# Kernel tuning notes

Hardware: AMD Instinct MI355X
Metric: run time of the kernel (lower is better)

The kernel has to match this reference:

```python
import jax, jax.numpy as jnp
import numpy as np

B, T, K, V, D, H = 16, 512, 32, 512, 64, 128


def setup_inputs() -> dict:
    key = jax.random.key(0)
    ks = jax.random.split(key, 10)
    s = lambda k, shape: jax.random.normal(k, shape, jnp.float32) * 0.05
    sequences = jax.random.randint(ks[0], (B, T), 0, V)
    lengths = jax.random.randint(ks[1], (B,), 1, T + 1)
    return dict(
        sequences=sequences,
        lengths=lengths,
        emb=s(ks[2], (V, D)),
        W1=s(ks[3], (D, H)), b1=jnp.zeros((H,), jnp.float32),
        W2=s(ks[4], (H, K * K)), b2=jnp.zeros((K * K,), jnp.float32),
        E1=s(ks[5], (D, H)), e1=jnp.zeros((H,), jnp.float32),
        E2=s(ks[6], (H, K * V)), e2=jnp.zeros((K * V,), jnp.float32),
        init_logits=s(ks[7], (K,)),
    )


def reference(sequences, lengths, emb, W1, b1, W2, b2, E1, e1, E2, e2, init_logits):
    Bc, Tc = sequences.shape
    # shift inputs: start token 0 followed by sequences[:, :-1]
    inputs = jnp.concatenate(
        [jnp.zeros((Bc, 1), sequences.dtype), sequences[:, :-1]], axis=1)
    x = emb[inputs]                                  # (B,T,D)
    # transition net -> (B,T,K,K) row-normalized in log space
    h1 = jax.nn.relu(x @ W1 + b1)
    log_trans = jax.nn.log_softmax((h1 @ W2 + b2).reshape(Bc, Tc, K, K), axis=-1)
    # emission net -> (B,T,K,V), gather observed-token scores
    h2 = jax.nn.relu(x @ E1 + e1)
    log_emit = jax.nn.log_softmax((h2 @ E2 + e2).reshape(Bc, Tc, K, V), axis=-1)
    tgt = jnp.broadcast_to(sequences[:, :, None, None], (Bc, Tc, K, 1))
    emit_scores = jnp.take_along_axis(log_emit, tgt, axis=3)[..., 0]  # (B,T,K)
    init_lp = jax.nn.log_softmax(init_logits)
    alpha0 = init_lp[None, :] + emit_scores[:, 0]    # (B,K)

    def step(alpha, xs):
        lt, es, t = xs                               # (B,K,K),(B,K),()
        new = jax.nn.logsumexp(alpha[:, :, None] + lt, axis=1) + es
        alpha = jnp.where((t < lengths)[:, None], new, alpha)
        return alpha, None

    xs = (jnp.swapaxes(log_trans, 0, 1)[1:],
          jnp.swapaxes(emit_scores, 0, 1)[1:],
          jnp.arange(1, Tc))
    alpha, _ = jax.lax.scan(step, alpha0, xs)
    return -jax.nn.logsumexp(alpha, axis=1)         # (B,) negative log-likelihood
```

## Files before the change

kernel.cpp:

```cpp
#include <hip/hip_runtime.h>
#include <hip/hip_bf16.h>

#define BB 16
#define TT 512
#define KK 32
#define VV 512
#define DD 64
#define HH 128
#define KV (KK*VV)
#define KKK (KK*KK)

#define INV_LN2 1.4426950408889634f
#define LN2 0.6931471805599453f

typedef unsigned short u16;
typedef __attribute__((ext_vector_type(8))) short short8;
typedef __attribute__((ext_vector_type(8))) unsigned short ushort8;
typedef __attribute__((ext_vector_type(16))) float f32x16;
typedef __attribute__((ext_vector_type(4))) unsigned int uint4v;

__device__ __forceinline__ float fexp2(float x) { return __builtin_amdgcn_exp2f(x); }
__device__ __forceinline__ float flog2(float x) { return __builtin_amdgcn_logf(x); }

__device__ __forceinline__ u16 f2bf(float f) {
  unsigned u = __builtin_bit_cast(unsigned, f);
  u += 0x7FFFu + ((u >> 16) & 1u);
  return (u16)(u >> 16);
}
__device__ __forceinline__ float bf2f(u16 v) {
  return __builtin_bit_cast(float, ((unsigned)v) << 16);
}

__device__ __forceinline__ float es_dot(const u16* __restrict__ erow,
                                        const u16* __restrict__ hrow) {
  float dot = 0.f;
#pragma unroll
  for (int r = 0; r < 8; ++r) {
    short8 ev = ((const short8*)erow)[r];
    short8 hv = ((const short8*)hrow)[r];
#pragma unroll
    for (int e = 0; e < 8; ++e)
      dot += bf2f((u16)ev[e]) * bf2f((u16)hv[e]);
  }
  return dot;
}

__device__ __forceinline__ void mul_step(short8 fr0, short8 fr1, int h,
                                         float* D) {
  float e0[8], e1[8];
#pragma unroll
  for (int i2 = 0; i2 < 4; ++i2) {
    float x0 = __shfl_xor(D[i2], 32);
    float y0 = __shfl_xor(D[4 + i2], 32);
    e0[i2] = (h == 0) ? D[i2] : y0;
    e0[4 + i2] = (h == 0) ? x0 : D[4 + i2];
    float x1 = __shfl_xor(D[8 + i2], 32);
    float y1 = __shfl_xor(D[12 + i2], 32);
    e1[i2] = (h == 0) ? D[8 + i2] : y1;
    e1[4 + i2] = (h == 0) ? x1 : D[12 + i2];
  }
  short8 B0, B1;
#pragma unroll
  for (int e = 0; e < 8; ++e) {
    B0[e] = (short)f2bf(e0[e]);
    B1[e] = (short)f2bf(e1[e]);
  }
  f32x16 dn = {};
  dn = __builtin_amdgcn_mfma_f32_32x32x16_bf16(fr0, B0, dn, 0, 0, 0);
  dn = __builtin_amdgcn_mfma_f32_32x32x16_bf16(fr1, B1, dn, 0, 0, 0);
#pragma unroll
  for (int r = 0; r < 16; ++r) D[r] = dn[r];
}

__device__ __forceinline__ void ident_D(int j, int h, float* D) {
#pragma unroll
  for (int r = 0; r < 16; ++r) D[r] = 0.f;
  if (((j >> 2) & 1) == h) D[(j & 3) | ((j >> 3) << 2)] = 1.0f;
}

__global__ __launch_bounds__(256) void k_prep(
    const float* __restrict__ E2, u16* __restrict__ E2bT,
    const float* __restrict__ emb, const float* __restrict__ W1,
    const float* __restrict__ b1, const float* __restrict__ E1,
    const float* __restrict__ e1, const float* __restrict__ W2,
    const float* __restrict__ b2, float* __restrict__ ltrans,
    u16* __restrict__ h2b) {
  __shared__ float tl[32][65];
  __shared__ float embs[4][64];
  __shared__ float h1s[4][128];
  __shared__ float lg[4][32 * 33];
  __shared__ float lsev[4][32];
  int tid = threadIdx.x;

  if (blockIdx.x < 1024) {
    int c0 = (blockIdx.x & 255) * 64, h0 = (blockIdx.x >> 8) * 32;
    int r = tid >> 6, c = tid & 63;
#pragma unroll
    for (int rr = 0; rr < 8; ++rr)
      tl[r * 8 + rr][c] = E2[(size_t)(h0 + r * 8 + rr) * KV + c0 + c];
    __syncthreads();
    int cw = tid >> 3, hb = tid & 7;
#pragma unroll
    for (int pass = 0; pass < 2; ++pass) {
      int cc = pass * 32 + cw;
      unsigned lo = (unsigned)f2bf(tl[hb * 4 + 0][cc]) |
                    ((unsigned)f2bf(tl[hb * 4 + 1][cc]) << 16);
      unsigned hi = (unsigned)f2bf(tl[hb * 4 + 2][cc]) |
                    ((unsigned)f2bf(tl[hb * 4 + 3][cc]) << 16);
      uint2 v;
      v.x = lo;
      v.y = hi;
      *(uint2*)(E2bT + (size_t)(c0 + cc) * HH + h0 + hb * 4) = v;
    }
    return;
  }

  int u0 = (blockIdx.x - 1024) * 4;
  {
    int tok = tid >> 6, d = tid & 63;
    embs[tok][d] = emb[(u0 + tok) * DD + d];
  }
  __syncthreads();
#pragma unroll
  for (int p = 0; p < 2; ++p) {
    int tok = p * 2 + (tid >> 7), hh = tid & 127;
    float a1 = b1[hh], a2 = e1[hh];
#pragma unroll 8
    for (int d = 0; d < DD; ++d) {
      float xv = embs[tok][d];
      a1 += xv * W1[d * HH + hh];
      a2 += xv * E1[d * HH + hh];
    }
    h1s[tok][hh] = fmaxf(a1, 0.f);
    h2b[(u0 + tok) * HH + hh] = f2bf(fmaxf(a2, 0.f));
  }
  __syncthreads();
  float acc[4][4];
#pragma unroll
  for (int r = 0; r < 4; ++r) {
    float bb = b2[tid + r * 256];
#pragma unroll
    for (int tok = 0; tok < 4; ++tok) acc[tok][r] = bb;
  }
#pragma unroll 2
  for (int hh = 0; hh < HH; ++hh) {
    float w0 = W2[hh * KKK + tid];
    float w1 = W2[hh * KKK + tid + 256];
    float w2v = W2[hh * KKK + tid + 512];
    float w3 = W2[hh * KKK + tid + 768];
#pragma unroll
    for (int tok = 0; tok < 4; ++tok) {
      float hv = h1s[tok][hh];
      acc[tok][0] += hv * w0;
      acc[tok][1] += hv * w1;
      acc[tok][2] += hv * w2v;
      acc[tok][3] += hv * w3;
    }
  }
#pragma unroll
  for (int tok = 0; tok < 4; ++tok)
#pragma unroll
    for (int r = 0; r < 4; ++r) {
      int cc = tid + r * 256;
      lg[tok][(cc >> 5) * 33 + (cc & 31)] = acc[tok][r] * INV_LN2;
    }
  __syncthreads();
  if (tid < 128) {
    int tok = tid >> 5, i = tid & 31;
    float m = -1e30f;
    for (int jj = 0; jj < KK; ++jj) m = fmaxf(m, lg[tok][i * 33 + jj]);
    float s = 0.f;
    for (int jj = 0; jj < KK; ++jj) s += fexp2(lg[tok][i * 33 + jj] - m);
    lsev[tok][i] = m + flog2(s);
  }
  __syncthreads();
#pragma unroll
  for (int tok = 0; tok < 4; ++tok)
#pragma unroll
    for (int r = 0; r < 4; ++r) {
      int cc = tid + r * 256;
      int jj = cc >> 5, ii = cc & 31;
      ltrans[(u0 + tok) * KKK + jj * KK + ii] =
          lg[tok][ii * 33 + jj] - lsev[tok][ii];
    }
}

__global__ __launch_bounds__(256) void k_emit_lse(
    const u16* __restrict__ h2b, const u16* __restrict__ E2bT,
    const float* __restrict__ e2, float* __restrict__ lse2_tab) {
  int k = blockIdx.x;
  int u0 = blockIdx.y * 32;
  int tid = threadIdx.x;
  int w = tid >> 6, l = tid & 63;
  int h = l >> 5, j = l & 31;
  __shared__ float ls[4 * 32];

  short8 A[8];
#pragma unroll
  for (int kh = 0; kh < 8; ++kh)
    A[kh] = *(const short8*)(h2b + (u0 + j) * HH + kh * 16 + h * 8);

  float s[16];
#pragma unroll
  for (int r = 0; r < 16; ++r) s[r] = 0.f;

#pragma unroll
  for (int c = 0; c < 4; ++c) {
    int ct = w * 4 + c;
    int col = k * 512 + ct * 32 + j;
    const u16* bp = E2bT + (size_t)col * HH + h * 8;
    f32x16 acc = {};
#pragma unroll
    for (int kh = 0; kh < 8; ++kh) {
      short8 Bf = *(const short8*)(bp + kh * 16);
      acc = __builtin_amdgcn_mfma_f32_32x32x16_bf16(A[kh], Bf, acc, 0, 0, 0);
    }
    float e2v = e2[col] * INV_LN2;
#pragma unroll
    for (int r = 0; r < 16; ++r) s[r] += fexp2(acc[r] * INV_LN2 + e2v);
  }
#pragma unroll
  for (int r = 0; r < 16; ++r) {
#pragma unroll
    for (int d = 1; d < 32; d <<= 1) s[r] += __shfl_xor(s[r], d);
  }
  if (j == 0) {
#pragma unroll
    for (int r = 0; r < 16; ++r) {
      int row = (r & 3) + 8 * (r >> 2) + 4 * h;
      ls[w * 32 + row] = s[r];
    }
  }
  __syncthreads();
  if (tid < 32) {
    float total = ls[tid] + ls[32 + tid] + ls[64 + tid] + ls[96 + tid];
    lse2_tab[(u0 + tid) * KK + k] = flog2(total);
  }
}

__global__ __launch_bounds__(256) void k_matprod(
    const int* __restrict__ seq, const int* __restrict__ lengths,
    const float* __restrict__ ltrans, const u16* __restrict__ h2b,
    const u16* __restrict__ E2bT, const float* __restrict__ e2,
    const float* __restrict__ lse2, u16* __restrict__ C1,
    float* __restrict__ s1) {
  __shared__ float tmp[4][32 * 33];
  int w = threadIdx.x >> 6, l = threadIdx.x & 63;
  int c = blockIdx.x * 4 + w;
  int b = c >> 6, t0 = (c & 63) * 8;
  int j = l & 31, h = l >> 5;
  int len = lengths[b];
  len = (len < 1) ? 1 : ((len > TT) ? TT : len);
  const int* sb = seq + b * TT;
  int tlo = (t0 < 1) ? 1 : t0;
  int thi = (t0 + 8 < len) ? (t0 + 8) : len;

  u16* op = C1 + (size_t)c * 1024 + j * 32 + h * 16;
  if (tlo >= thi) {
    ushort8 w0v, w1v;
#pragma unroll
    for (int e = 0; e < 8; ++e) {
      w0v[e] = ((h * 16 + e) == j) ? (u16)0x3F80 : (u16)0;
      w1v[e] = ((h * 16 + 8 + e) == j) ? (u16)0x3F80 : (u16)0;
    }
    *(ushort8*)op = w0v;
    *(ushort8*)(op + 8) = w1v;
    if (l == 0) s1[c] = 0.f;
    return;
  }

  short8 fr0s[8], fr1s[8];
  float sacc = 0.f;
#pragma unroll
  for (int s = 0; s < 8; ++s) {
    int t = t0 + s;
    if (t >= 1 && t < len) {
      int u = sb[t - 1], y = sb[t];
      float dot = es_dot(E2bT + (size_t)(j * VV + y) * HH + h * 64,
                         h2b + u * HH + h * 64);
      dot += __shfl_xor(dot, 32);
      float esj = (dot + e2[j * VV + y]) * INV_LN2 - lse2[u * KK + j];
      float m = esj;
#pragma unroll
      for (int d = 1; d < 32; d <<= 1) m = fmaxf(m, __shfl_xor(m, d));
      sacc += m;
      const float4* p4 = (const float4*)(ltrans + u * KKK + j * KK + h * 16);
      float4 q0 = p4[0], q1 = p4[1], q2 = p4[2], q3 = p4[3];
      float lgv[16] = {q0.x, q0.y, q0.z, q0.w, q1.x, q1.y, q1.z, q1.w,
                       q2.x, q2.y, q2.z, q2.w, q3.x, q3.y, q3.z, q3.w};
      float off = esj - m;
#pragma unroll
      for (int e = 0; e < 16; ++e) lgv[e] += off;
      unsigned pk[8];
#pragma unroll
      for (int p = 0; p < 8; ++p)
        pk[p] = (unsigned)f2bf(fexp2(lgv[2 * p])) |
                ((unsigned)f2bf(fexp2(lgv[2 * p + 1])) << 16);
      unsigned rcv[4];
#pragma unroll
      for (int p = 0; p < 4; ++p)
        rcv[p] = (unsigned)__shfl_xor((int)(h == 0 ? pk[4 + p] : pk[p]), 32);
      unsigned f0[4], f1[4];
#pragma unroll
      for (int p = 0; p < 4; ++p) {
        f0[p] = h == 0 ? pk[p] : rcv[p];
        f1[p] = h == 0 ? rcv[p] : pk[4 + p];
      }
      fr0s[s] = __builtin_bit_cast(short8, (uint4v){f0[0], f0[1], f0[2], f0[3]});
      fr1s[s] = __builtin_bit_cast(short8, (uint4v){f1[0], f1[1], f1[2], f1[3]});
    } else {
      ushort8 i0, i1;
#pragma unroll
      for (int e = 0; e < 8; ++e) {
        i0[e] = ((h * 8 + e) == j) ? (u16)0x3F80 : (u16)0;
        i1[e] = ((16 + h * 8 + e) == j) ? (u16)0x3F80 : (u16)0;
      }
      fr0s[s] = __builtin_bit_cast(short8, i0);
      fr1s[s] = __builtin_bit_cast(short8, i1);
    }
  }

  float D[16];
  ident_D(j, h, D);
#pragma unroll
  for (int s = 0; s < 8; ++s) mul_step(fr0s[s], fr1s[s], h, D);

  float mx = D[0];
#pragma unroll
  for (int r = 1; r < 16; ++r) mx = fmaxf(mx, D[r]);
#pragma unroll
  for (int d = 1; d < 64; d <<= 1) mx = fmaxf(mx, __shfl_xor(mx, d));
  float inv = 1.0f / mx;
#pragma unroll
  for (int r = 0; r < 16; ++r) {
    int row = (r & 3) + 8 * (r >> 2) + 4 * h;
    tmp[w][row * 33 + j] = D[r] * inv;
  }
  ushort8 w0v, w1v;
#pragma unroll
  for (int e = 0; e < 8; ++e) {
    w0v[e] = f2bf(tmp[w][j * 33 + h * 16 + e]);
    w1v[e] = f2bf(tmp[w][j * 33 + h * 16 + 8 + e]);
  }
  *(ushort8*)op = w0v;
  *(ushort8*)(op + 8) = w1v;
  if (l == 0) s1[c] = flog2(mx) + sacc;
}

__global__ __launch_bounds__(512) void k_final2(
    const u16* __restrict__ C1, const float* __restrict__ s1,
    const int* __restrict__ seq, const u16* __restrict__ h2b,
    const u16* __restrict__ E2bT, const float* __restrict__ e2,
    const float* __restrict__ lse2, const float* __restrict__ init_logits,
    float* __restrict__ out) {
  __shared__ u16 mats[8][1024];
  __shared__ float scs[8];
  int b = blockIdx.x;
  int w = threadIdx.x >> 6, l = threadIdx.x & 63;
  int j = l & 31, h = l >> 5;

  float D[16];
  ident_D(j, h, D);
  const u16* base = C1 + ((size_t)b * 64 + w * 8) * 1024;
#pragma unroll
  for (int s = 0; s < 8; ++s) {
    short8 fr0 = *(const short8*)(base + s * 1024 + j * 32 + h * 8);
    short8 fr1 = *(const short8*)(base + s * 1024 + j * 32 + h * 8 + 16);
    mul_step(fr0, fr1, h, D);
  }
  float mx = D[0];
#pragma unroll
  for (int r = 1; r < 16; ++r) mx = fmaxf(mx, D[r]);
#pragma unroll
  for (int d = 1; d < 64; d <<= 1) mx = fmaxf(mx, __shfl_xor(mx, d));
  float inv = 1.0f / mx;
#pragma unroll
  for (int r = 0; r < 16; ++r) {
    int row = (r & 3) + 8 * (r >> 2) + 4 * h;
    mats[w][row * 32 + j] = f2bf(D[r] * inv);
  }
  float si = (l < 8) ? s1[b * 64 + w * 8 + l] : 0.f;
#pragma unroll
  for (int d = 1; d < 64; d <<= 1) si += __shfl_xor(si, d);
  if (l == 0) scs[w] = flog2(mx) + si;
  __syncthreads();

  if (w == 0) {
    float D2[16];
    ident_D(j, h, D2);
#pragma unroll
    for (int s = 0; s < 8; ++s) {
      short8 fr0 = *(const short8*)(&mats[s][j * 32 + h * 8]);
      short8 fr1 = *(const short8*)(&mats[s][j * 32 + h * 8 + 16]);
      mul_step(fr0, fr1, h, D2);
    }
    int y0 = seq[b * TT];
    float dot = es_dot(E2bT + (size_t)(j * VV + y0) * HH + h * 64,
                       h2b + h * 64);
    dot += __shfl_xor(dot, 32);
    float esj = (dot + e2[j * VV + y0]) * INV_LN2 - lse2[j];
    float il = init_logits[j] * INV_LN2;
    float m0 = il;
#pragma unroll
    for (int d = 1; d < 32; d <<= 1) m0 = fmaxf(m0, __shfl_xor(m0, d));
    float s0 = fexp2(il - m0);
#pragma unroll
    for (int d = 1; d < 32; d <<= 1) s0 += __shfl_xor(s0, d);
    float lse0 = m0 + flog2(s0);
    float z = il - lse0 + esj;
    float am = z;
#pragma unroll
    for (int d = 1; d < 32; d <<= 1) am = fmaxf(am, __shfl_xor(am, d));
    float a0 = fexp2(z - am);
    float colsum = 0.f;
#pragma unroll
    for (int r = 0; r < 16; ++r) colsum += D2[r];
    float p = a0 * colsum;
#pragma unroll
    for (int d = 1; d < 64; d <<= 1) p += __shfl_xor(p, d);
    float sct = (l < 8) ? scs[l] : 0.f;
#pragma unroll
    for (int d = 1; d < 64; d <<= 1) sct += __shfl_xor(sct, d);
    if (l == 0) out[b] = -LN2 * (flog2(p) + am + sct);
  }
}

extern "C" void kernel_launch(void* const* d_in, const int* in_sizes, int n_in,
                              void* d_out, int out_size, void* d_ws,
                              size_t ws_size, hipStream_t stream) {
  const int* seq = (const int*)d_in[0];
  const int* lengths = (const int*)d_in[1];
  const float* emb = (const float*)d_in[2];
  const float* W1 = (const float*)d_in[3];
  const float* b1 = (const float*)d_in[4];
  const float* W2 = (const float*)d_in[5];
  const float* b2 = (const float*)d_in[6];
  const float* E1 = (const float*)d_in[7];
  const float* e1 = (const float*)d_in[8];
  const float* E2 = (const float*)d_in[9];
  const float* e2 = (const float*)d_in[10];
  const float* init_logits = (const float*)d_in[11];
  float* out = (float*)d_out;

  char* wsb = (char*)d_ws;
  float* ltrans = (float*)(wsb + 0);
  u16* h2b = (u16*)(wsb + 2097152);
  u16* E2bT = (u16*)(wsb + 2228224);
  float* lse2 = (float*)(wsb + 6422528);
  u16* C1 = (u16*)(wsb + 6488064);
  float* s1 = (float*)(wsb + 8585216);

  k_prep<<<1152, 256, 0, stream>>>(E2, E2bT, emb, W1, b1, E1, e1, W2, b2,
                                   ltrans, h2b);
  k_emit_lse<<<dim3(32, 16), 256, 0, stream>>>(h2b, E2bT, e2, lse2);
  k_matprod<<<256, 256, 0, stream>>>(seq, lengths, ltrans, h2b, E2bT, e2,
                                     lse2, C1, s1);
  k_final2<<<16, 512, 0, stream>>>(C1, s1, seq, h2b, E2bT, e2, lse2,
                                   init_logits, out);
}
```

Measured before the change: 88.56 us.

## Compute transition logits with MFMA and rebalance matprod chunk length

The fp32 scalar W2 projection and log-softmax in the prep kernel are replaced by a new MFMA kernel working on bf16 h1 and a transposed bf16 W2, with the row log-sum-exp done through wave shuffles. The prep kernel now also transposes W2 and processes 16 tokens per block for the first-layer MLPs. The matprod chunk shrinks from 8 to 4 steps, doubling its blocks, while the final kernel multiplies 16 chunk matrices per wave instead of 8. The es_dot reduction gains four independent accumulators. In exchange this adds a kernel launch, lowers transition precision to bf16 inputs, and lengthens the serial chain in the final kernel.

```diff
diff --git a/kernel.cpp b/kernel.cpp
--- a/kernel.cpp
+++ b/kernel.cpp
@@ -33,16 +33,21 @@
 
 __device__ __forceinline__ float es_dot(const u16* __restrict__ erow,
                                         const u16* __restrict__ hrow) {
-  float dot = 0.f;
+  float a0 = 0.f, a1 = 0.f, a2 = 0.f, a3 = 0.f;
 #pragma unroll
   for (int r = 0; r < 8; ++r) {
     short8 ev = ((const short8*)erow)[r];
     short8 hv = ((const short8*)hrow)[r];
-#pragma unroll
-    for (int e = 0; e < 8; ++e)
-      dot += bf2f((u16)ev[e]) * bf2f((u16)hv[e]);
-  }
-  return dot;
+    a0 += bf2f((u16)ev[0]) * bf2f((u16)hv[0]);
+    a1 += bf2f((u16)ev[1]) * bf2f((u16)hv[1]);
+    a2 += bf2f((u16)ev[2]) * bf2f((u16)hv[2]);
+    a3 += bf2f((u16)ev[3]) * bf2f((u16)hv[3]);
+    a0 += bf2f((u16)ev[4]) * bf2f((u16)hv[4]);
+    a1 += bf2f((u16)ev[5]) * bf2f((u16)hv[5]);
+    a2 += bf2f((u16)ev[6]) * bf2f((u16)hv[6]);
+    a3 += bf2f((u16)ev[7]) * bf2f((u16)hv[7]);
+  }
+  return (a0 + a1) + (a2 + a3);
 }
 
 __device__ __forceinline__ void mul_step(short8 fr0, short8 fr1, int h,
@@ -78,26 +83,41 @@
   if (((j >> 2) & 1) == h) D[(j & 3) | ((j >> 3) << 2)] = 1.0f;
 }
 
-__global__ __launch_bounds__(256) void k_prep(
+__global__ __launch_bounds__(256) void k_prep1(
     const float* __restrict__ E2, u16* __restrict__ E2bT,
+    const float* __restrict__ W2, u16* __restrict__ W2T,
     const float* __restrict__ emb, const float* __restrict__ W1,
     const float* __restrict__ b1, const float* __restrict__ E1,
-    const float* __restrict__ e1, const float* __restrict__ W2,
-    const float* __restrict__ b2, float* __restrict__ ltrans,
+    const float* __restrict__ e1, u16* __restrict__ h1b,
     u16* __restrict__ h2b) {
   __shared__ float tl[32][65];
-  __shared__ float embs[4][64];
-  __shared__ float h1s[4][128];
-  __shared__ float lg[4][32 * 33];
-  __shared__ float lsev[4][32];
+  __shared__ float embs[16][64];
   int tid = threadIdx.x;
-
-  if (blockIdx.x < 1024) {
-    int c0 = (blockIdx.x & 255) * 64, h0 = (blockIdx.x >> 8) * 32;
+  int bid = blockIdx.x;
+
+  if (bid < 1088) {
+    const float* src;
+    u16* dst;
+    size_t srcld;
+    int c0, h0;
+    if (bid < 1024) {
+      c0 = (bid & 255) * 64;
+      h0 = (bid >> 8) * 32;
+      src = E2;
+      dst = E2bT;
+      srcld = KV;
+    } else {
+      int b2i = bid - 1024;
+      c0 = (b2i & 15) * 64;
+      h0 = (b2i >> 4) * 32;
+      src = W2;
+      dst = W2T;
+      srcld = KKK;
+    }
     int r = tid >> 6, c = tid & 63;
 #pragma unroll
     for (int rr = 0; rr < 8; ++rr)
-      tl[r * 8 + rr][c] = E2[(size_t)(h0 + r * 8 + rr) * KV + c0 + c];
+      tl[r * 8 + rr][c] = src[(size_t)(h0 + r * 8 + rr) * srcld + c0 + c];
     __syncthreads();
     int cw = tid >> 3, hb = tid & 7;
 #pragma unroll
@@ -110,79 +130,68 @@
       uint2 v;
       v.x = lo;
       v.y = hi;
-      *(uint2*)(E2bT + (size_t)(c0 + cc) * HH + h0 + hb * 4) = v;
+      *(uint2*)(dst + (size_t)(c0 + cc) * HH + h0 + hb * 4) = v;
     }
     return;
   }
 
-  int u0 = (blockIdx.x - 1024) * 4;
-  {
-    int tok = tid >> 6, d = tid & 63;
-    embs[tok][d] = emb[(u0 + tok) * DD + d];
+  int u0 = (bid - 1088) * 16;
+#pragma unroll
+  for (int it = 0; it < 4; ++it) {
+    int idx = it * 256 + tid;
+    embs[idx >> 6][idx & 63] = emb[u0 * DD + idx];
   }
   __syncthreads();
-#pragma unroll
-  for (int p = 0; p < 2; ++p) {
-    int tok = p * 2 + (tid >> 7), hh = tid & 127;
-    float a1 = b1[hh], a2 = e1[hh];
+  int h = tid & 127, tl2 = tid >> 7;
+  float b1v = b1[h], e1v = e1[h];
+#pragma unroll
+  for (int it = 0; it < 8; ++it) {
+    int tok = it * 2 + tl2;
+    float a1 = b1v, a2 = e1v;
 #pragma unroll 8
     for (int d = 0; d < DD; ++d) {
       float xv = embs[tok][d];
-      a1 += xv * W1[d * HH + hh];
-      a2 += xv * E1[d * HH + hh];
-    }
-    h1s[tok][hh] = fmaxf(a1, 0.f);
-    h2b[(u0 + tok) * HH + hh] = f2bf(fmaxf(a2, 0.f));
-  }
-  __syncthreads();
-  float acc[4][4];
-#pragma unroll
-  for (int r = 0; r < 4; ++r) {
-    float bb = b2[tid + r * 256];
-#pragma unroll
-    for (int tok = 0; tok < 4; ++tok) acc[tok][r] = bb;
-  }
-#pragma unroll 2
-  for (int hh = 0; hh < HH; ++hh) {
-    float w0 = W2[hh * KKK + tid];
-    float w1 = W2[hh * KKK + tid + 256];
-    float w2v = W2[hh * KKK + tid + 512];
-    float w3 = W2[hh * KKK + tid + 768];
-#pragma unroll
-    for (int tok = 0; tok < 4; ++tok) {
-      float hv = h1s[tok][hh];
-      acc[tok][0] += hv * w0;
-      acc[tok][1] += hv * w1;
-      acc[tok][2] += hv * w2v;
-      acc[tok][3] += hv * w3;
-    }
-  }
-#pragma unroll
-  for (int tok = 0; tok < 4; ++tok)
-#pragma unroll
-    for (int r = 0; r < 4; ++r) {
-      int cc = tid + r * 256;
-      lg[tok][(cc >> 5) * 33 + (cc & 31)] = acc[tok][r] * INV_LN2;
-    }
-  __syncthreads();
-  if (tid < 128) {
-    int tok = tid >> 5, i = tid & 31;
-    float m = -1e30f;
-    for (int jj = 0; jj < KK; ++jj) m = fmaxf(m, lg[tok][i * 33 + jj]);
-    float s = 0.f;
-    for (int jj = 0; jj < KK; ++jj) s += fexp2(lg[tok][i * 33 + jj] - m);
-    lsev[tok][i] = m + flog2(s);
-  }
-  __syncthreads();
-#pragma unroll
-  for (int tok = 0; tok < 4; ++tok)
-#pragma unroll
-    for (int r = 0; r < 4; ++r) {
-      int cc = tid + r * 256;
-      int jj = cc >> 5, ii = cc & 31;
-      ltrans[(u0 + tok) * KKK + jj * KK + ii] =
-          lg[tok][ii * 33 + jj] - lsev[tok][ii];
-    }
+      a1 += xv * W1[d * HH + h];
+      a2 += xv * E1[d * HH + h];
+    }
+    h1b[(u0 + tok) * HH + h] = f2bf(fmaxf(a1, 0.f));
+    h2b[(u0 + tok) * HH + h] = f2bf(fmaxf(a2, 0.f));
+  }
+}
+
+__global__ __launch_bounds__(256) void k_transmfma(
+    const u16* __restrict__ h1b, const u16* __restrict__ W2T,
+    const float* __restrict__ b2, float* __restrict__ ltrans) {
+  int i = blockIdx.x;
+  int w = threadIdx.x >> 6, l = threadIdx.x & 63;
+  int tt = blockIdx.y * 4 + w;
+  int u0 = tt * 32;
+  int h = l >> 5, j = l & 31;
+
+  f32x16 acc = {};
+#pragma unroll
+  for (int kh = 0; kh < 8; ++kh) {
+    short8 A = *(const short8*)(h1b + (u0 + j) * HH + kh * 16 + h * 8);
+    short8 Bf = *(const short8*)(W2T + (i * 32 + j) * HH + kh * 16 + h * 8);
+    acc = __builtin_amdgcn_mfma_f32_32x32x16_bf16(A, Bf, acc, 0, 0, 0);
+  }
+  float b2v = b2[i * 32 + j] * INV_LN2;
+  float lgv[16], se[16];
+#pragma unroll
+  for (int r = 0; r < 16; ++r) {
+    lgv[r] = acc[r] * INV_LN2 + b2v;
+    se[r] = fexp2(lgv[r]);
+  }
+#pragma unroll
+  for (int r = 0; r < 16; ++r) {
+#pragma unroll
+    for (int d = 1; d < 32; d <<= 1) se[r] += __shfl_xor(se[r], d);
+  }
+#pragma unroll
+  for (int r = 0; r < 16; ++r) {
+    int row = (r & 3) + 8 * (r >> 2) + 4 * h;
+    ltrans[(u0 + row) * KKK + j * KK + i] = lgv[r] - flog2(se[r]);
+  }
 }
 
 __global__ __launch_bounds__(256) void k_emit_lse(
@@ -247,13 +256,13 @@
   __shared__ float tmp[4][32 * 33];
   int w = threadIdx.x >> 6, l = threadIdx.x & 63;
   int c = blockIdx.x * 4 + w;
-  int b = c >> 6, t0 = (c & 63) * 8;
+  int b = c >> 7, t0 = (c & 127) * 4;
   int j = l & 31, h = l >> 5;
   int len = lengths[b];
   len = (len < 1) ? 1 : ((len > TT) ? TT : len);
   const int* sb = seq + b * TT;
   int tlo = (t0 < 1) ? 1 : t0;
-  int thi = (t0 + 8 < len) ? (t0 + 8) : len;
+  int thi = (t0 + 4 < len) ? (t0 + 4) : len;
 
   u16* op = C1 + (size_t)c * 1024 + j * 32 + h * 16;
   if (tlo >= thi) {
@@ -269,10 +278,10 @@
     return;
   }
 
-  short8 fr0s[8], fr1s[8];
+  short8 fr0s[4], fr1s[4];
   float sacc = 0.f;
 #pragma unroll
-  for (int s = 0; s < 8; ++s) {
+  for (int s = 0; s < 4; ++s) {
     int t = t0 + s;
     if (t >= 1 && t < len) {
       int u = sb[t - 1], y = sb[t];
@@ -323,7 +332,7 @@
   float D[16];
   ident_D(j, h, D);
 #pragma unroll
-  for (int s = 0; s < 8; ++s) mul_step(fr0s[s], fr1s[s], h, D);
+  for (int s = 0; s < 4; ++s) mul_step(fr0s[s], fr1s[s], h, D);
 
   float mx = D[0];
 #pragma unroll
@@ -361,9 +370,9 @@
 
   float D[16];
   ident_D(j, h, D);
-  const u16* base = C1 + ((size_t)b * 64 + w * 8) * 1024;
-#pragma unroll
-  for (int s = 0; s < 8; ++s) {
+  const u16* base = C1 + ((size_t)b * 128 + w * 16) * 1024;
+#pragma unroll
+  for (int s = 0; s < 16; ++s) {
     short8 fr0 = *(const short8*)(base + s * 1024 + j * 32 + h * 8);
     short8 fr1 = *(const short8*)(base + s * 1024 + j * 32 + h * 8 + 16);
     mul_step(fr0, fr1, h, D);
@@ -379,7 +388,7 @@
     int row = (r & 3) + 8 * (r >> 2) + 4 * h;
     mats[w][row * 32 + j] = f2bf(D[r] * inv);
   }
-  float si = (l < 8) ? s1[b * 64 + w * 8 + l] : 0.f;
+  float si = (l < 16) ? s1[b * 128 + w * 16 + l] : 0.f;
 #pragma unroll
   for (int d = 1; d < 64; d <<= 1) si += __shfl_xor(si, d);
   if (l == 0) scs[w] = flog2(mx) + si;
@@ -445,15 +454,18 @@
   char* wsb = (char*)d_ws;
   float* ltrans = (float*)(wsb + 0);
   u16* h2b = (u16*)(wsb + 2097152);
-  u16* E2bT = (u16*)(wsb + 2228224);
-  float* lse2 = (float*)(wsb + 6422528);
-  u16* C1 = (u16*)(wsb + 6488064);
-  float* s1 = (float*)(wsb + 8585216);
-
-  k_prep<<<1152, 256, 0, stream>>>(E2, E2bT, emb, W1, b1, E1, e1, W2, b2,
-                                   ltrans, h2b);
+  u16* h1b = (u16*)(wsb + 2228224);
+  u16* E2bT = (u16*)(wsb + 2359296);
+  u16* W2T = (u16*)(wsb + 6553600);
+  float* lse2 = (float*)(wsb + 6815744);
+  u16* C1 = (u16*)(wsb + 6881280);
+  float* s1 = (float*)(wsb + 11075584);
+
+  k_prep1<<<1120, 256, 0, stream>>>(E2, E2bT, W2, W2T, emb, W1, b1, E1, e1,
+                                    h1b, h2b);
+  k_transmfma<<<dim3(32, 4), 256, 0, stream>>>(h1b, W2T, b2, ltrans);
   k_emit_lse<<<dim3(32, 16), 256, 0, stream>>>(h2b, E2bT, e2, lse2);
-  k_matprod<<<256, 256, 0, stream>>>(seq, lengths, ltrans, h2b, E2bT, e2,
+  k_matprod<<<512, 256, 0, stream>>>(seq, lengths, ltrans, h2b, E2bT, e2,
                                      lse2, C1, s1);
   k_final2<<<16, 512, 0, stream>>>(C1, s1, seq, h2b, E2bT, e2, lse2,
                                    init_logits, out);
```

Result: no change. 90.32 us (+2.0%).
